# Performance work log

Hardware: AMD Instinct MI355X
Metric: run time of the kernel (lower is better)

Reference implementation:

```python
import jax, jax.numpy as jnp
import numpy as np
from jax import lax

Q = 3          # Self-ONN polynomial order
EPS = 1e-5     # InstanceNorm1d eps


def setup_inputs() -> dict:
    key = jax.random.key(0)
    k1, k2, k3 = jax.random.split(key, 3)
    B, Cin, L = 16, 128, 8192
    Cout, K = 128, 3
    x = jax.random.normal(k1, (B, Cin, L), dtype=jnp.float32)
    # Conv1d weight over power-expanded channels: [Cout, Cin*Q, K]
    W = jax.random.normal(k2, (Cout, Cin * Q, K), dtype=jnp.float32) * 0.05
    b = jax.random.normal(k3, (Cout,), dtype=jnp.float32) * 0.05
    return {"x": x, "W": W, "b": b}


def reference(x, W, b):
    x = jnp.repeat(x, 2, axis=-1)
    # Self-ONN power expansion: concat x^1..x^Q along channel dim -> (B, C*Q, 2L)
    powers = jnp.concatenate([x ** (i + 1) for i in range(Q)], axis=1)
    # Conv1d, stride 1, padding 1 (same length)
    out = lax.conv_general_dilated(
        powers, W,
        window_strides=(1,),
        padding=[(1, 1)],
        dimension_numbers=("NCH", "OIH", "NCH"),
    ) + b[None, :, None]
    # InstanceNorm1d (affine=False): normalize over length per (batch, channel)
    mean = jnp.mean(out, axis=-1, keepdims=True)
    var = jnp.var(out, axis=-1, keepdims=True)
    out = (out - mean) * lax.rsqrt(var + EPS)
    # Tanh activation (self.relu is nn.Tanh()); dropout=False -> no-op
    return jnp.tanh(out)
```

## Files before the change

### kernel.cpp

```cpp
#include <hip/hip_runtime.h>
#include <hip/hip_fp16.h>
#include <math.h>

#define BATCH 16
#define CIN   128
#define LIN   8192
#define COUT  128
#define LOUT  16384
#define KEXP  768
#define NT    128
#define NTILES (LIN/NT)
#define PCOLS 130
#define PCPAD 136
#define PSZ   (PCOLS*PCPAD)

typedef _Float16 f16x8 __attribute__((ext_vector_type(8)));
typedef float    f32x4 __attribute__((ext_vector_type(4)));

__global__ void prep_weights(const float* __restrict__ W,
                             _Float16* __restrict__ WE,
                             _Float16* __restrict__ WO) {
  int idx = blockIdx.x * 256 + threadIdx.x;
  int co = idx / KEXP;
  int k  = idx % KEXP;
  int sh = (k >= 384) ? 1 : 0;
  int cq = k - 384 * sh;
  const float* w = W + ((size_t)co * 384 + cq) * 3;
  float we, wo;
  if (sh == 0) { we = w[0];        wo = w[0] + w[1]; }
  else         { we = w[1] + w[2]; wo = w[2];        }
  int q  = cq >> 7;
  int c  = cq & 127;
  int ks = q * 8 + sh * 4 + (c >> 5);
  int kk = c & 31, quad = kk >> 3, j = kk & 7;
  int mtile = co >> 4, l15 = co & 15;
  size_t off = ((size_t)((mtile * 24 + ks) * 64) + quad * 16 + l15) * 8 + j;
  WE[off] = (_Float16)we;
  WO[off] = (_Float16)wo;
}


#define BUILD_PLANE(POW, P) do {                                           \
  _Pragma("unroll")                                                        \
  for (int slot = 0; slot < 5; ++slot) {                                   \
    if (slot < 4 || tail) {                                                \
      f16x8 w;                                                             \
      _Pragma("unroll")                                                    \
      for (int j = 0; j < 8; ++j) {                                        \
        float v = xv[slot][j];                                             \
        float pv = ((POW) == 1) ? v : (((POW) == 2) ? v * v : v * (v * v));\
        w[j] = (_Float16)pv;                                               \
      }                                                                    \
      *(f16x8*)((P) + woff[slot]) = w;                                     \
    }                                                                      \
  }                                                                        \
} while (0)

#define AFLOAD(DST, KS) do {                                               \
  _Pragma("unroll")                                                        \
  for (int fm = 0; fm < 4; ++fm) {                                         \
    int mt = wm * 4 + fm;                                                  \
    DST[fm] = *(const f16x8*)(Wsel + ((size_t)((mt * 24 + (KS)) * 64) + lane) * 8); \
  }                                                                        \
} while (0)

#define BFLOAD(DST, CUR, S) do {                                           \
  _Pragma("unroll")                                                        \
  for (int fn = 0; fn < 4; ++fn) {                                         \
    int colB = wn * 64 + fn * 16 + l15 + (((S) >> 2) + isO);               \
    DST[fn] = *(const f16x8*)((CUR) + colB * PCPAD + ((S) & 3) * 32 + kl); \
  }                                                                        \
} while (0)

__launch_bounds__(512, 2)
__global__ void conv_gemm(const float* __restrict__ x,
                          const _Float16* __restrict__ WE,
                          const _Float16* __restrict__ WO,
                          float* __restrict__ out,
                          float* __restrict__ stats) {
  extern __shared__ char smem[];
  float*    sstats = (float*)smem;
  _Float16* planes = (_Float16*)(smem + 1024);

  const int tile = blockIdx.x;
  const int b    = blockIdx.y;
  const int i0   = tile * NT;
  const int t    = threadIdx.x;
  const int lane = t & 63;
  const int wave = t >> 6;
  const int p    = wave >> 1;
  const int isO  = wave & 1;
  const int wm   = p >> 1, wn = p & 1;
  const int l15  = lane & 15, quad = lane >> 4;
  const int kl   = quad * 8;

  if (t < 128) { sstats[2 * t] = 0.f; sstats[2 * t + 1] = 0.f; }

  const float* xb = x + (size_t)b * CIN * LIN;
  const _Float16* Wsel = isO ? WO : WE;

  float xv[5][8];
  int   woff[5];
  const bool tail = (t < PCOLS * 16 - 2048);
#pragma unroll
  for (int slot = 0; slot < 5; ++slot) {
    const bool tval = (slot < 4) || tail;
    int task = t + 512 * slot;
    int g    = task / PCOLS;
    if (!tval) g = 0;
    int col  = task - g * PCOLS;
    int gi   = i0 - 1 + col;
    woff[slot] = col * PCPAD + g * 8;
    const bool ok = tval && gi >= 0 && gi < LIN;
    const float* px = xb + (size_t)g * 8 * LIN + gi;
#pragma unroll
    for (int j = 0; j < 8; ++j) {
      float v = 0.f;
      if (ok) v = px[(size_t)j * LIN];
      xv[slot][j] = v;
    }
  }

  f32x4 acc[4][4];
  const f32x4 zero = {0.f, 0.f, 0.f, 0.f};
#pragma unroll
  for (int fm = 0; fm < 4; ++fm)
#pragma unroll
    for (int fn = 0; fn < 4; ++fn) acc[fm][fn] = zero;

  f16x8 af[3][4], bf[2][4];
  AFLOAD(af[0], 0);
  AFLOAD(af[1], 1);
  BUILD_PLANE(1, planes);
  __syncthreads();

#pragma unroll
  for (int q = 0; q < 3; ++q) {
    _Float16* cur = planes + (size_t)(q & 1) * PSZ;
    BFLOAD(bf[0], cur, 0);
    if (q == 0)      BUILD_PLANE(2, planes + PSZ);
    else if (q == 1) BUILD_PLANE(3, planes);

#pragma unroll
    for (int s = 0; s < 8; ++s) {
      const int ks = q * 8 + s;
      if (ks + 2 < 24) AFLOAD(af[(ks + 2) % 3], ks + 2);
      if (s < 7)       BFLOAD(bf[(s + 1) & 1], cur, s + 1);
      __builtin_amdgcn_s_setprio(1);
#pragma unroll
      for (int fm = 0; fm < 4; ++fm)
#pragma unroll
        for (int fn = 0; fn < 4; ++fn)
          acc[fm][fn] = __builtin_amdgcn_mfma_f32_16x16x32_f16(af[ks % 3][fm], bf[s & 1][fn], acc[fm][fn], 0, 0, 0);
      __builtin_amdgcn_s_setprio(0);
    }
    __syncthreads();
  }

  float* orow_base = out + (size_t)b * COUT * LOUT + isO;
#pragma unroll
  for (int fm = 0; fm < 4; ++fm) {
#pragma unroll
    for (int r = 0; r < 4; ++r) {
      float s1 = 0.f, s2 = 0.f;
#pragma unroll
      for (int fn = 0; fn < 4; ++fn) {
        float v = acc[fm][fn][r];
        s1 += v;
        s2 += v * v;
      }
#pragma unroll
      for (int off = 8; off >= 1; off >>= 1) {
        s1 += __shfl_xor(s1, off, 64);
        s2 += __shfl_xor(s2, off, 64);
      }
      int co = wm * 64 + fm * 16 + quad * 4 + r;
      if (l15 == 0) {
        atomicAdd(&sstats[2 * co], s1);
        atomicAdd(&sstats[2 * co + 1], s2);
      }
      float* orow = orow_base + (size_t)co * LOUT;
#pragma unroll
      for (int fn = 0; fn < 4; ++fn) {
        int n = i0 + wn * 64 + fn * 16 + l15;
        orow[2 * n] = acc[fm][fn][r];
      }
    }
  }
  __syncthreads();
  if (t < 128) {
    atomicAdd(&stats[((size_t)b * COUT + t) * 2],     sstats[2 * t]);
    atomicAdd(&stats[((size_t)b * COUT + t) * 2 + 1], sstats[2 * t + 1]);
  }
}

__device__ inline float tanh_fast(float z) {
  float e = __expf(2.f * z);
  return 1.f - 2.f * __builtin_amdgcn_rcpf(e + 1.f);
}

__global__ void norm_tanh(float* __restrict__ out, const float* __restrict__ stats) {
  int row = blockIdx.x;
  float s1 = stats[2 * row], s2 = stats[2 * row + 1];
  const float invN = 1.f / (float)LOUT;
  float mean = s1 * invN;
  float var  = fmaxf(s2 * invN - mean * mean, 0.f);
  float inv  = rsqrtf(var + 1e-5f);
  float c0   = -mean * inv;
  float4* p = (float4*)(out + (size_t)row * LOUT);
  for (int i = threadIdx.x; i < LOUT / 4; i += 256) {
    float4 v = p[i];
    v.x = tanh_fast(fmaf(v.x, inv, c0));
    v.y = tanh_fast(fmaf(v.y, inv, c0));
    v.z = tanh_fast(fmaf(v.z, inv, c0));
    v.w = tanh_fast(fmaf(v.w, inv, c0));
    p[i] = v;
  }
}

extern "C" void kernel_launch(void* const* d_in, const int* in_sizes, int n_in,
                              void* d_out, int out_size, void* d_ws, size_t ws_size,
                              hipStream_t stream) {
  const float* x = (const float*)d_in[0];
  const float* W = (const float*)d_in[1];
  float* out = (float*)d_out;

  float*    stats = (float*)d_ws;
  _Float16* WE    = (_Float16*)((char*)d_ws + 16384);
  _Float16* WO    = WE + (size_t)COUT * KEXP;

  hipMemsetAsync(d_ws, 0, 16384, stream);
  prep_weights<<<dim3((COUT * KEXP) / 256), dim3(256), 0, stream>>>(W, WE, WO);

  size_t shmem = 1024 + (size_t)PSZ * 2 * 2;
  hipFuncSetAttribute(reinterpret_cast<const void*>(conv_gemm),
                      hipFuncAttributeMaxDynamicSharedMemorySize, (int)shmem);
  conv_gemm<<<dim3(NTILES, BATCH), dim3(512), shmem, stream>>>(x, WE, WO, out, stats);

  norm_tanh<<<dim3(BATCH * COUT), dim3(256), 0, stream>>>(out, stats);
}
```

Before: 276.5 us.

## Halve conv tile to 64 columns and build all three power planes upfront

The tile width drops from 128 to 64 input columns and the block shrinks from 512 to 256 threads (4 waves, no N split). All three power planes (x, x^2, x^3) are written to LDS once before a single barrier, instead of double-buffering and interleaving plane construction with the MFMA loop. The K loop becomes one flat 24-step loop with no intermediate syncs. This doubles the grid size and removes two barriers per block. In exchange, each block now loads weights for half as many columns, so weight traffic per output roughly doubles, and LDS per block grows to three planes.

Result: slower. 282.4 us (+2.1%).

```diff
diff --git a/kernel.cpp b/kernel.cpp
--- a/kernel.cpp
+++ b/kernel.cpp
@@ -8,9 +8,9 @@
 #define COUT  128
 #define LOUT  16384
 #define KEXP  768
-#define NT    128
+#define NT    64
 #define NTILES (LIN/NT)
-#define PCOLS 130
+#define PCOLS 66
 #define PCPAD 136
 #define PSZ   (PCOLS*PCPAD)
 
@@ -40,22 +40,6 @@
 }
 
 
-#define BUILD_PLANE(POW, P) do {                                           \
-  _Pragma("unroll")                                                        \
-  for (int slot = 0; slot < 5; ++slot) {                                   \
-    if (slot < 4 || tail) {                                                \
-      f16x8 w;                                                             \
-      _Pragma("unroll")                                                    \
-      for (int j = 0; j < 8; ++j) {                                        \
-        float v = xv[slot][j];                                             \
-        float pv = ((POW) == 1) ? v : (((POW) == 2) ? v * v : v * (v * v));\
-        w[j] = (_Float16)pv;                                               \
-      }                                                                    \
-      *(f16x8*)((P) + woff[slot]) = w;                                     \
-    }                                                                      \
-  }                                                                        \
-} while (0)
-
 #define AFLOAD(DST, KS) do {                                               \
   _Pragma("unroll")                                                        \
   for (int fm = 0; fm < 4; ++fm) {                                         \
@@ -64,15 +48,18 @@
   }                                                                        \
 } while (0)
 
-#define BFLOAD(DST, CUR, S) do {                                           \
+#define BFLOAD(DST, KS) do {                                               \
+  const _Float16* pb = planes + (size_t)((KS) >> 3) * PSZ                  \
+                       + (((KS) & 3) * 32) + kl;                           \
+  const int shft = ((((KS) & 7) >> 2) + isO);                              \
   _Pragma("unroll")                                                        \
   for (int fn = 0; fn < 4; ++fn) {                                         \
-    int colB = wn * 64 + fn * 16 + l15 + (((S) >> 2) + isO);               \
-    DST[fn] = *(const f16x8*)((CUR) + colB * PCPAD + ((S) & 3) * 32 + kl); \
+    int colB = fn * 16 + l15 + shft;                                       \
+    DST[fn] = *(const f16x8*)(pb + colB * PCPAD);                          \
   }                                                                        \
 } while (0)
 
-__launch_bounds__(512, 2)
+__launch_bounds__(256, 2)
 __global__ void conv_gemm(const float* __restrict__ x,
                           const _Float16* __restrict__ WE,
                           const _Float16* __restrict__ WO,
@@ -88,9 +75,8 @@
   const int t    = threadIdx.x;
   const int lane = t & 63;
   const int wave = t >> 6;
-  const int p    = wave >> 1;
+  const int wm   = wave >> 1;
   const int isO  = wave & 1;
-  const int wm   = p >> 1, wn = p & 1;
   const int l15  = lane & 15, quad = lane >> 4;
   const int kl   = quad * 8;
 
@@ -99,25 +85,30 @@
   const float* xb = x + (size_t)b * CIN * LIN;
   const _Float16* Wsel = isO ? WO : WE;
 
-  float xv[5][8];
-  int   woff[5];
-  const bool tail = (t < PCOLS * 16 - 2048);
+  const bool tail = (t < PCOLS * 16 - 1024);
 #pragma unroll
   for (int slot = 0; slot < 5; ++slot) {
     const bool tval = (slot < 4) || tail;
-    int task = t + 512 * slot;
+    int task = t + 256 * slot;
     int g    = task / PCOLS;
-    if (!tval) g = 0;
     int col  = task - g * PCOLS;
     int gi   = i0 - 1 + col;
-    woff[slot] = col * PCPAD + g * 8;
     const bool ok = tval && gi >= 0 && gi < LIN;
     const float* px = xb + (size_t)g * 8 * LIN + gi;
+    f16x8 w1, w2, w3;
 #pragma unroll
     for (int j = 0; j < 8; ++j) {
-      float v = 0.f;
-      if (ok) v = px[(size_t)j * LIN];
-      xv[slot][j] = v;
+      float v  = ok ? px[(size_t)j * LIN] : 0.f;
+      float v2 = v * v;
+      w1[j] = (_Float16)v;
+      w2[j] = (_Float16)v2;
+      w3[j] = (_Float16)(v2 * v);
+    }
+    if (tval) {
+      int off = col * PCPAD + g * 8;
+      *(f16x8*)(planes + off)           = w1;
+      *(f16x8*)(planes + PSZ + off)     = w2;
+      *(f16x8*)(planes + 2 * PSZ + off) = w3;
     }
   }
 
@@ -131,30 +122,20 @@
   f16x8 af[3][4], bf[2][4];
   AFLOAD(af[0], 0);
   AFLOAD(af[1], 1);
-  BUILD_PLANE(1, planes);
   __syncthreads();
-
-#pragma unroll
-  for (int q = 0; q < 3; ++q) {
-    _Float16* cur = planes + (size_t)(q & 1) * PSZ;
-    BFLOAD(bf[0], cur, 0);
-    if (q == 0)      BUILD_PLANE(2, planes + PSZ);
-    else if (q == 1) BUILD_PLANE(3, planes);
-
-#pragma unroll
-    for (int s = 0; s < 8; ++s) {
-      const int ks = q * 8 + s;
-      if (ks + 2 < 24) AFLOAD(af[(ks + 2) % 3], ks + 2);
-      if (s < 7)       BFLOAD(bf[(s + 1) & 1], cur, s + 1);
-      __builtin_amdgcn_s_setprio(1);
-#pragma unroll
-      for (int fm = 0; fm < 4; ++fm)
-#pragma unroll
-        for (int fn = 0; fn < 4; ++fn)
-          acc[fm][fn] = __builtin_amdgcn_mfma_f32_16x16x32_f16(af[ks % 3][fm], bf[s & 1][fn], acc[fm][fn], 0, 0, 0);
-      __builtin_amdgcn_s_setprio(0);
-    }
-    __syncthreads();
+  BFLOAD(bf[0], 0);
+
+#pragma unroll
+  for (int ks = 0; ks < 24; ++ks) {
+    if (ks + 2 < 24) AFLOAD(af[(ks + 2) % 3], ks + 2);
+    if (ks + 1 < 24) BFLOAD(bf[(ks + 1) & 1], ks + 1);
+    __builtin_amdgcn_s_setprio(1);
+#pragma unroll
+    for (int fm = 0; fm < 4; ++fm)
+#pragma unroll
+      for (int fn = 0; fn < 4; ++fn)
+        acc[fm][fn] = __builtin_amdgcn_mfma_f32_16x16x32_f16(af[ks % 3][fm], bf[ks & 1][fn], acc[fm][fn], 0, 0, 0);
+    __builtin_amdgcn_s_setprio(0);
   }
 
   float* orow_base = out + (size_t)b * COUT * LOUT + isO;
@@ -182,7 +163,7 @@
       float* orow = orow_base + (size_t)co * LOUT;
 #pragma unroll
       for (int fn = 0; fn < 4; ++fn) {
-        int n = i0 + wn * 64 + fn * 16 + l15;
+        int n = i0 + fn * 16 + l15;
         orow[2 * n] = acc[fm][fn][r];
       }
     }
@@ -232,10 +213,10 @@
   hipMemsetAsync(d_ws, 0, 16384, stream);
   prep_weights<<<dim3((COUT * KEXP) / 256), dim3(256), 0, stream>>>(W, WE, WO);
 
-  size_t shmem = 1024 + (size_t)PSZ * 2 * 2;
+  size_t shmem = 1024 + (size_t)PSZ * 3 * 2;
   hipFuncSetAttribute(reinterpret_cast<const void*>(conv_gemm),
                       hipFuncAttributeMaxDynamicSharedMemorySize, (int)shmem);
-  conv_gemm<<<dim3(NTILES, BATCH), dim3(512), shmem, stream>>>(x, WE, WO, out, stats);
+  conv_gemm<<<dim3(NTILES, BATCH), dim3(256), shmem, stream>>>(x, WE, WO, out, stats);
 
   norm_tanh<<<dim3(BATCH * COUT), dim3(256), 0, stream>>>(out, stats);
 }
```

## Double N tile per block, build power planes from fp16 in LDS, split norm rows

Applied to the files above, without the earlier changes.

Doubles the sequence tile per workgroup to 256 columns, so each wave computes a 64x128 output sub-tile with 32 accumulators. This raises reuse of the weight fragments and halves the number of blocks. The x^2 and x^3 planes are now computed from the fp16 x plane already in shared memory, after the first MFMA step, instead of holding raw fp32 x in registers. The A prefetch depth drops from 3 buffers to 2, and norm_tanh launches two blocks per row. The costs are higher register pressure (128 accumulator floats per thread) and about 140KB of LDS, which likely limits occupancy to one block per CU. Computing the powers in fp16 also loses some precision.

New measurement: 328.7 us. 18.9% more time.

```diff
diff --git a/kernel.cpp b/kernel.cpp
--- a/kernel.cpp
+++ b/kernel.cpp
@@ -8,9 +8,9 @@
 #define COUT  128
 #define LOUT  16384
 #define KEXP  768
-#define NT    128
+#define NT    256
 #define NTILES (LIN/NT)
-#define PCOLS 130
+#define PCOLS 258
 #define PCPAD 136
 #define PSZ   (PCOLS*PCPAD)
 
@@ -40,22 +40,6 @@
 }
 
 
-#define BUILD_PLANE(POW, P) do {                                           \
-  _Pragma("unroll")                                                        \
-  for (int slot = 0; slot < 5; ++slot) {                                   \
-    if (slot < 4 || tail) {                                                \
-      f16x8 w;                                                             \
-      _Pragma("unroll")                                                    \
-      for (int j = 0; j < 8; ++j) {                                        \
-        float v = xv[slot][j];                                             \
-        float pv = ((POW) == 1) ? v : (((POW) == 2) ? v * v : v * (v * v));\
-        w[j] = (_Float16)pv;                                               \
-      }                                                                    \
-      *(f16x8*)((P) + woff[slot]) = w;                                     \
-    }                                                                      \
-  }                                                                        \
-} while (0)
-
 #define AFLOAD(DST, KS) do {                                               \
   _Pragma("unroll")                                                        \
   for (int fm = 0; fm < 4; ++fm) {                                         \
@@ -65,10 +49,41 @@
 } while (0)
 
 #define BFLOAD(DST, CUR, S) do {                                           \
-  _Pragma("unroll")                                                        \
-  for (int fn = 0; fn < 4; ++fn) {                                         \
-    int colB = wn * 64 + fn * 16 + l15 + (((S) >> 2) + isO);               \
-    DST[fn] = *(const f16x8*)((CUR) + colB * PCPAD + ((S) & 3) * 32 + kl); \
+  const _Float16* pb = (CUR) + (((S) & 3) * 32) + kl;                      \
+  const int shft = (((S) >> 2) + isO);                                     \
+  _Pragma("unroll")                                                        \
+  for (int fn = 0; fn < 8; ++fn) {                                         \
+    int colB = wn * 128 + fn * 16 + l15 + shft;                            \
+    DST[fn] = *(const f16x8*)(pb + colB * PCPAD);                          \
+  }                                                                        \
+} while (0)
+
+#define BUILD_P2() do {                                                    \
+  _Pragma("unroll")                                                        \
+  for (int slot = 0; slot < 9; ++slot) {                                   \
+    if (slot < 8 || t < PCOLS * 16 - 4096) {                               \
+      int task = t + 512 * slot;                                           \
+      int g    = task / PCOLS;                                             \
+      int col  = task - g * PCOLS;                                         \
+      int off  = col * PCPAD + g * 8;                                      \
+      f16x8 v = *(f16x8*)(planes + off);                                   \
+      *(f16x8*)(planes + PSZ + off) = v * v;                               \
+    }                                                                      \
+  }                                                                        \
+} while (0)
+
+#define BUILD_P3() do {                                                    \
+  _Pragma("unroll")                                                        \
+  for (int slot = 0; slot < 9; ++slot) {                                   \
+    if (slot < 8 || t < PCOLS * 16 - 4096) {                               \
+      int task = t + 512 * slot;                                           \
+      int g    = task / PCOLS;                                             \
+      int col  = task - g * PCOLS;                                         \
+      int off  = col * PCPAD + g * 8;                                      \
+      f16x8 v1 = *(f16x8*)(planes + off);                                  \
+      f16x8 v2 = *(f16x8*)(planes + PSZ + off);                            \
+      *(f16x8*)(planes + off) = v1 * v2;                                   \
+    }                                                                      \
   }                                                                        \
 } while (0)
 
@@ -88,9 +103,9 @@
   const int t    = threadIdx.x;
   const int lane = t & 63;
   const int wave = t >> 6;
-  const int p    = wave >> 1;
   const int isO  = wave & 1;
-  const int wm   = p >> 1, wn = p & 1;
+  const int wn   = (wave >> 1) & 1;
+  const int wm   = wave >> 2;
   const int l15  = lane & 15, quad = lane >> 4;
   const int kl   = quad * 8;
 
@@ -99,60 +114,53 @@
   const float* xb = x + (size_t)b * CIN * LIN;
   const _Float16* Wsel = isO ? WO : WE;
 
-  float xv[5][8];
-  int   woff[5];
-  const bool tail = (t < PCOLS * 16 - 2048);
-#pragma unroll
-  for (int slot = 0; slot < 5; ++slot) {
-    const bool tval = (slot < 4) || tail;
+  f32x4 acc[4][8];
+  const f32x4 zero = {0.f, 0.f, 0.f, 0.f};
+#pragma unroll
+  for (int fm = 0; fm < 4; ++fm)
+#pragma unroll
+    for (int fn = 0; fn < 8; ++fn) acc[fm][fn] = zero;
+
+  f16x8 af[2][4], bf[2][8];
+  AFLOAD(af[0], 0);
+
+#pragma unroll
+  for (int slot = 0; slot < 9; ++slot) {
+    const bool tval = (slot < 8) || (t < PCOLS * 16 - 4096);
     int task = t + 512 * slot;
     int g    = task / PCOLS;
-    if (!tval) g = 0;
     int col  = task - g * PCOLS;
     int gi   = i0 - 1 + col;
-    woff[slot] = col * PCPAD + g * 8;
     const bool ok = tval && gi >= 0 && gi < LIN;
     const float* px = xb + (size_t)g * 8 * LIN + gi;
+    f16x8 w1;
 #pragma unroll
     for (int j = 0; j < 8; ++j) {
-      float v = 0.f;
-      if (ok) v = px[(size_t)j * LIN];
-      xv[slot][j] = v;
+      float v = ok ? px[(size_t)j * LIN] : 0.f;
+      w1[j] = (_Float16)v;
     }
-  }
-
-  f32x4 acc[4][4];
-  const f32x4 zero = {0.f, 0.f, 0.f, 0.f};
-#pragma unroll
-  for (int fm = 0; fm < 4; ++fm)
-#pragma unroll
-    for (int fn = 0; fn < 4; ++fn) acc[fm][fn] = zero;
-
-  f16x8 af[3][4], bf[2][4];
-  AFLOAD(af[0], 0);
-  AFLOAD(af[1], 1);
-  BUILD_PLANE(1, planes);
+    if (tval) *(f16x8*)(planes + col * PCPAD + g * 8) = w1;
+  }
   __syncthreads();
 
 #pragma unroll
   for (int q = 0; q < 3; ++q) {
-    _Float16* cur = planes + (size_t)(q & 1) * PSZ;
+    _Float16* cur = planes + ((q == 1) ? PSZ : 0);
     BFLOAD(bf[0], cur, 0);
-    if (q == 0)      BUILD_PLANE(2, planes + PSZ);
-    else if (q == 1) BUILD_PLANE(3, planes);
-
 #pragma unroll
     for (int s = 0; s < 8; ++s) {
       const int ks = q * 8 + s;
-      if (ks + 2 < 24) AFLOAD(af[(ks + 2) % 3], ks + 2);
-      if (s < 7)       BFLOAD(bf[(s + 1) & 1], cur, s + 1);
+      if (ks + 1 < 24) AFLOAD(af[(ks + 1) & 1], ks + 1);
+      if (s + 1 < 8)   BFLOAD(bf[(s + 1) & 1], cur, s + 1);
       __builtin_amdgcn_s_setprio(1);
 #pragma unroll
       for (int fm = 0; fm < 4; ++fm)
 #pragma unroll
-        for (int fn = 0; fn < 4; ++fn)
-          acc[fm][fn] = __builtin_amdgcn_mfma_f32_16x16x32_f16(af[ks % 3][fm], bf[s & 1][fn], acc[fm][fn], 0, 0, 0);
+        for (int fn = 0; fn < 8; ++fn)
+          acc[fm][fn] = __builtin_amdgcn_mfma_f32_16x16x32_f16(af[ks & 1][fm], bf[s & 1][fn], acc[fm][fn], 0, 0, 0);
       __builtin_amdgcn_s_setprio(0);
+      if (s == 0 && q == 0) BUILD_P2();
+      if (s == 0 && q == 1) BUILD_P3();
     }
     __syncthreads();
   }
@@ -164,7 +172,7 @@
     for (int r = 0; r < 4; ++r) {
       float s1 = 0.f, s2 = 0.f;
 #pragma unroll
-      for (int fn = 0; fn < 4; ++fn) {
+      for (int fn = 0; fn < 8; ++fn) {
         float v = acc[fm][fn][r];
         s1 += v;
         s2 += v * v;
@@ -181,8 +189,8 @@
       }
       float* orow = orow_base + (size_t)co * LOUT;
 #pragma unroll
-      for (int fn = 0; fn < 4; ++fn) {
-        int n = i0 + wn * 64 + fn * 16 + l15;
+      for (int fn = 0; fn < 8; ++fn) {
+        int n = i0 + wn * 128 + fn * 16 + l15;
         orow[2 * n] = acc[fm][fn][r];
       }
     }
@@ -200,15 +208,16 @@
 }
 
 __global__ void norm_tanh(float* __restrict__ out, const float* __restrict__ stats) {
-  int row = blockIdx.x;
+  int row  = blockIdx.x >> 1;
+  int half = blockIdx.x & 1;
   float s1 = stats[2 * row], s2 = stats[2 * row + 1];
   const float invN = 1.f / (float)LOUT;
   float mean = s1 * invN;
   float var  = fmaxf(s2 * invN - mean * mean, 0.f);
   float inv  = rsqrtf(var + 1e-5f);
   float c0   = -mean * inv;
-  float4* p = (float4*)(out + (size_t)row * LOUT);
-  for (int i = threadIdx.x; i < LOUT / 4; i += 256) {
+  float4* p = (float4*)(out + (size_t)row * LOUT) + half * (LOUT / 8);
+  for (int i = threadIdx.x; i < LOUT / 8; i += 256) {
     float4 v = p[i];
     v.x = tanh_fast(fmaf(v.x, inv, c0));
     v.y = tanh_fast(fmaf(v.y, inv, c0));
@@ -237,5 +246,5 @@
                       hipFuncAttributeMaxDynamicSharedMemorySize, (int)shmem);
   conv_gemm<<<dim3(NTILES, BATCH), dim3(512), shmem, stream>>>(x, WE, WO, out, stats);
 
-  norm_tanh<<<dim3(BATCH * COUT), dim3(256), 0, stream>>>(out, stats);
-}
+  norm_tanh<<<dim3(2 * BATCH * COUT), dim3(256), 0, stream>>>(out, stats);
+}
```
